# Optimization experiments

Measured on AMD Instinct MI355X. Metric: run time of the kernel, lower is better.

## Reference

```python
import jax, jax.numpy as jnp
import numpy as np

INPUT, HIDDEN, OUTPUT = 512, 1024, 512
B, T = 256, 512

def setup_inputs() -> dict:
    key = jax.random.key(0)
    ks = jax.random.split(key, 15)
    def lin(k, fin, fout):
        bound = 1.0 / np.sqrt(fin)
        kw, kb = jax.random.split(k)
        W = jax.random.uniform(kw, (fout, fin), jnp.float32, -bound, bound)
        b = jax.random.uniform(kb, (fout,), jnp.float32, -bound, bound)
        return W, b
    x = jax.random.normal(ks[0], (B, T, INPUT), jnp.float32)
    Wxr, bxr = lin(ks[1], INPUT, HIDDEN)
    Whr, bhr = lin(ks[2], HIDDEN, HIDDEN)
    Wxc, bxc = lin(ks[3], INPUT, HIDDEN)
    Whc, bhc = lin(ks[4], HIDDEN, HIDDEN)
    Wxz, bxz = lin(ks[5], INPUT, HIDDEN)
    Whz, bhz = lin(ks[6], HIDDEN, HIDDEN)
    Wo, bo = lin(ks[7], HIDDEN, OUTPUT)
    return {"x": x, "Wxr": Wxr, "bxr": bxr, "Whr": Whr, "bhr": bhr,
            "Wxc": Wxc, "bxc": bxc, "Whc": Whc, "bhc": bhc,
            "Wxz": Wxz, "bxz": bxz, "Whz": Whz, "bhz": bhz,
            "Wo": Wo, "bo": bo}

def reference(x, Wxr, bxr, Whr, bhr, Wxc, bxc, Whc, bhc, Wxz, bxz, Whz, bhz, Wo, bo):
    # Precompute all input-to-gate projections in one big GEMM each: [B,T,H]
    xr = jnp.einsum('bti,hi->bth', x, Wxr) + bxr
    xc = jnp.einsum('bti,hi->bth', x, Wxc) + bxc
    xz = jnp.einsum('bti,hi->bth', x, Wxz) + bxz
    # time-major for scan: [T,B,H]
    xs = (xr.transpose(1, 0, 2), xc.transpose(1, 0, 2), xz.transpose(1, 0, 2))

    h0 = jnp.zeros((x.shape[0], Whr.shape[0]), x.dtype)

    def step(h, xt):
        xr_t, xc_t, xz_t = xt
        r = jax.nn.sigmoid(xr_t + h @ Whr.T + bhr)
        c = jnp.tanh(xc_t + r * (h @ Whc.T + bhc))
        z = jax.nn.sigmoid(xz_t + h @ Whz.T + bhz)
        h_new = (1.0 - z) * h + z * c
        return h_new, None

    h_final, _ = jax.lax.scan(step, h0, xs)
    return h_final @ Wo.T + bo
```

## Files before the change

kernel.cpp:

```cpp
#include <hip/hip_runtime.h>

typedef __attribute__((ext_vector_type(8))) short s16x8;
typedef __attribute__((ext_vector_type(4))) float f32x4;

#define SCOPE_AGENT __HIP_MEMORY_SCOPE_AGENT

static __device__ __forceinline__ unsigned short f2bf(float f) {
    unsigned u = __float_as_uint(f);
    u = (u + 0x7fffu + ((u >> 16) & 1u)) >> 16;
    return (unsigned short)u;
}

static __device__ __forceinline__ unsigned ld_sc1(const unsigned* p) {
    return __hip_atomic_load(p, __ATOMIC_RELAXED, SCOPE_AGENT);
}
static __device__ __forceinline__ void st_sc1(unsigned* p, unsigned v) {
    __hip_atomic_store(p, v, __ATOMIC_RELAXED, SCOPE_AGENT);
}

__global__ void k_cast_bf16(const float* __restrict__ src,
                            unsigned short* __restrict__ dst, int n4) {
    int i = blockIdx.x * blockDim.x + threadIdx.x;
    int stride = gridDim.x * blockDim.x;
    for (; i < n4; i += stride) {
        float4 v = reinterpret_cast<const float4*>(src)[i];
        ushort4 o;
        o.x = f2bf(v.x); o.y = f2bf(v.y); o.z = f2bf(v.z); o.w = f2bf(v.w);
        reinterpret_cast<ushort4*>(dst)[i] = o;
    }
}

__global__ __launch_bounds__(256, 1) void k_gru(
    const unsigned short* __restrict__ x16,
    const unsigned short* __restrict__ wh,
    const unsigned short* __restrict__ wx,
    const unsigned short* __restrict__ wo,
    const float* __restrict__ bxr_, const float* __restrict__ bhr_,
    const float* __restrict__ bxc_, const float* __restrict__ bhc_,
    const float* __restrict__ bxz_, const float* __restrict__ bhz_,
    const float* __restrict__ bo_,
    unsigned short* __restrict__ h16a,
    unsigned short* __restrict__ h16b,
    unsigned* __restrict__ slots,
    unsigned* __restrict__ rel,
    float* __restrict__ out)
{
    extern __shared__ unsigned short lds[];

    const int tid = threadIdx.x;
    const int bid = blockIdx.x;
    const int xcd = bid & 7;
    const int rb  = xcd >> 1;
    const int jt  = ((bid >> 3) << 1) | (xcd & 1);
    const int b0  = rb * 64;
    const int j0  = jt * 16;

    for (int i = 0; i < 36; ++i) {
        int gidx = i * 256 + tid;
        int rr = gidx / 192;
        int gc = gidx - rr * 192;
        int k  = gc << 3;
        int gate = rr >> 4;
        int j = j0 + (rr & 15);
        const unsigned short* src =
            (k < 1024) ? (wh + ((size_t)gate << 20) + ((size_t)j << 10) + k)
                       : (wx + (size_t)gate * 524288 + ((size_t)j << 9) + (k - 1024));
        s16x8 v = *reinterpret_cast<const s16x8*>(src);
        int boff = ((rr * 192 + gc) << 4) ^ ((rr & 7) << 4);
        *reinterpret_cast<s16x8*>(reinterpret_cast<char*>(lds) + boff) = v;
    }
    __syncthreads();

    const int lane = tid & 63;
    const int wv   = tid >> 6;
    const int l15  = lane & 15;
    const int lk   = lane >> 4;

    const int b   = b0 + wv * 16 + l15;
    const int jq  = j0 + lk * 4;
    const int swz = (l15 & 7) << 4;
    const int rbase0 = (l15)      * 192 + lk;
    const int rbase1 = (16 + l15) * 192 + lk;
    const int rbase2 = (32 + l15) * 192 + lk;

    float bR[4], bZ[4], bCh[4], bCx[4];
#pragma unroll
    for (int e = 0; e < 4; ++e) {
        int j = jq + e;
        bR[e]  = bxr_[j] + bhr_[j];
        bZ[e]  = bxz_[j] + bhz_[j];
        bCh[e] = bhc_[j];
        bCx[e] = bxc_[j];
    }

    float hreg[4] = {0.f, 0.f, 0.f, 0.f};
    char* lb = reinterpret_cast<char*>(lds);
    const unsigned short* xrowbase = x16 + (size_t)b * 262144 + lk * 8;
    unsigned* myflag  = &slots[(rb << 6) + jt];
    unsigned* grel    = &rel[rb << 6];

    f32x4 xR = {0.f,0.f,0.f,0.f}, xZ = {0.f,0.f,0.f,0.f}, xC = {0.f,0.f,0.f,0.f};
    {
        s16x8 xf[16];
#pragma unroll
        for (int kk = 0; kk < 16; ++kk)
            xf[kk] = *reinterpret_cast<const s16x8*>(xrowbase + kk * 32);
#pragma unroll
        for (int kk = 0; kk < 16; ++kk) {
            s16x8 w0 = *reinterpret_cast<s16x8*>(lb + (((rbase0 + (kk + 32) * 4) << 4) ^ swz));
            s16x8 w1 = *reinterpret_cast<s16x8*>(lb + (((rbase1 + (kk + 32) * 4) << 4) ^ swz));
            s16x8 w2 = *reinterpret_cast<s16x8*>(lb + (((rbase2 + (kk + 32) * 4) << 4) ^ swz));
            xR = __builtin_amdgcn_mfma_f32_16x16x32_bf16(w0, xf[kk], xR, 0, 0, 0);
            xC = __builtin_amdgcn_mfma_f32_16x16x32_bf16(w1, xf[kk], xC, 0, 0, 0);
            xZ = __builtin_amdgcn_mfma_f32_16x16x32_bf16(w2, xf[kk], xZ, 0, 0, 0);
        }
    }

    unsigned short* hc = h16a;
    unsigned short* hn = h16b;

    for (int t = 0; t < 512; ++t) {
        if (wv == 0) {
            while (ld_sc1(grel) < (unsigned)t) __builtin_amdgcn_s_sleep(1);
        }
        __syncthreads();
        asm volatile("" ::: "memory");

        s16x8 hf[32];
        const unsigned short* hrow = hc + ((size_t)b << 10) + lk * 8;
#pragma unroll
        for (int kk = 0; kk < 32; ++kk)
            hf[kk] = *reinterpret_cast<const s16x8*>(hrow + kk * 32);

        s16x8 xfn[16];
        if (t < 511) {
            const unsigned short* axn = xrowbase + (size_t)(t + 1) * 512;
#pragma unroll
            for (int kk = 0; kk < 16; ++kk)
                xfn[kk] = *reinterpret_cast<const s16x8*>(axn + kk * 32);
        }

        f32x4 aR = xR, aZ = xZ, aCx = xC;
        f32x4 aCh = {0.f,0.f,0.f,0.f};
#pragma unroll
        for (int kk = 0; kk < 32; ++kk) {
            s16x8 w0 = *reinterpret_cast<s16x8*>(lb + (((rbase0 + kk * 4) << 4) ^ swz));
            s16x8 w1 = *reinterpret_cast<s16x8*>(lb + (((rbase1 + kk * 4) << 4) ^ swz));
            s16x8 w2 = *reinterpret_cast<s16x8*>(lb + (((rbase2 + kk * 4) << 4) ^ swz));
            aR  = __builtin_amdgcn_mfma_f32_16x16x32_bf16(w0, hf[kk], aR, 0, 0, 0);
            aCh = __builtin_amdgcn_mfma_f32_16x16x32_bf16(w1, hf[kk], aCh, 0, 0, 0);
            aZ  = __builtin_amdgcn_mfma_f32_16x16x32_bf16(w2, hf[kk], aZ, 0, 0, 0);
        }

        unsigned long long pack = 0ull;
#pragma unroll
        for (int e = 0; e < 4; ++e) {
            float r   = __builtin_amdgcn_rcpf(1.f + __expf(-(aR[e] + bR[e])));
            float zg  = __builtin_amdgcn_rcpf(1.f + __expf(-(aZ[e] + bZ[e])));
            float u2  = aCx[e] + bCx[e] + r * (aCh[e] + bCh[e]);
            float cg  = 1.f - 2.f * __builtin_amdgcn_rcpf(__expf(2.f * u2) + 1.f);
            float hnv = (1.f - zg) * hreg[e] + zg * cg;
            hreg[e] = hnv;
            pack |= (unsigned long long)f2bf(hnv) << (16 * e);
        }
        __hip_atomic_store(
            reinterpret_cast<unsigned long long*>(hn + ((size_t)b << 10) + jq),
            pack, __ATOMIC_RELAXED, SCOPE_AGENT);

        __syncthreads();
        if (tid == 0) {
            st_sc1(myflag, (unsigned)(t + 1));
            (void)__hip_atomic_load(grel, __ATOMIC_ACQUIRE, SCOPE_AGENT);
        }

        if (jt == 0 && wv == 0) {
            const unsigned tgt = (unsigned)(t + 1);
            for (;;) {
                unsigned v = ld_sc1(&slots[(rb << 6) + lane]);
                if (__all((int)(v >= tgt))) break;
                __builtin_amdgcn_s_sleep(1);
            }
            if (tid == 0) st_sc1(grel, tgt);
        }

        if (t < 511) {
            xR = {0.f,0.f,0.f,0.f}; xZ = {0.f,0.f,0.f,0.f}; xC = {0.f,0.f,0.f,0.f};
#pragma unroll
            for (int kk = 0; kk < 16; ++kk) {
                s16x8 w0 = *reinterpret_cast<s16x8*>(lb + (((rbase0 + (kk + 32) * 4) << 4) ^ swz));
                s16x8 w1 = *reinterpret_cast<s16x8*>(lb + (((rbase1 + (kk + 32) * 4) << 4) ^ swz));
                s16x8 w2 = *reinterpret_cast<s16x8*>(lb + (((rbase2 + (kk + 32) * 4) << 4) ^ swz));
                xR = __builtin_amdgcn_mfma_f32_16x16x32_bf16(w0, xfn[kk], xR, 0, 0, 0);
                xC = __builtin_amdgcn_mfma_f32_16x16x32_bf16(w1, xfn[kk], xC, 0, 0, 0);
                xZ = __builtin_amdgcn_mfma_f32_16x16x32_bf16(w2, xfn[kk], xZ, 0, 0, 0);
            }
        }

        unsigned short* tmp = hc; hc = hn; hn = tmp;
    }

    if (wv == 0) {
        while (ld_sc1(grel) < 512u) __builtin_amdgcn_s_sleep(1);
        (void)__hip_atomic_load(grel, __ATOMIC_ACQUIRE, SCOPE_AGENT);
    }
    __syncthreads();
    asm volatile("" ::: "memory");

    const int ocol  = jt * 8 + l15;
    const int ocolc = (l15 < 8) ? ocol : (jt * 8 + 7);
    f32x4 aO = {0.f,0.f,0.f,0.f};
    const unsigned short* hrow = hc + ((size_t)b << 10) + lk * 8;
    const unsigned short* bw = wo + ((size_t)ocolc << 10) + lk * 8;
#pragma unroll
    for (int kk = 0; kk < 32; ++kk) {
        s16x8 hv = *reinterpret_cast<const s16x8*>(hrow + kk * 32);
        s16x8 wb = *reinterpret_cast<const s16x8*>(bw + kk * 32);
        aO = __builtin_amdgcn_mfma_f32_16x16x32_bf16(hv, wb, aO, 0, 0, 0);
    }
    if (l15 < 8) {
        const float bov = bo_[ocol];
#pragma unroll
        for (int e = 0; e < 4; ++e) {
            out[((size_t)(b0 + wv * 16 + lk * 4 + e) << 9) + ocol] = aO[e] + bov;
        }
    }
}

extern "C" void kernel_launch(void* const* d_in, const int* in_sizes, int n_in,
                              void* d_out, int out_size, void* d_ws, size_t ws_size,
                              hipStream_t stream) {
    const float* x   = (const float*)d_in[0];
    const float* Wxr = (const float*)d_in[1];
    const float* bxr = (const float*)d_in[2];
    const float* Whr = (const float*)d_in[3];
    const float* bhr = (const float*)d_in[4];
    const float* Wxc = (const float*)d_in[5];
    const float* bxc = (const float*)d_in[6];
    const float* Whc = (const float*)d_in[7];
    const float* bhc = (const float*)d_in[8];
    const float* Wxz = (const float*)d_in[9];
    const float* bxz = (const float*)d_in[10];
    const float* Whz = (const float*)d_in[11];
    const float* bhz = (const float*)d_in[12];
    const float* Wo  = (const float*)d_in[13];
    const float* bo  = (const float*)d_in[14];

    char* ws = (char*)d_ws;
    unsigned short* x16  = (unsigned short*)(ws);
    unsigned short* wh   = (unsigned short*)(ws + 134217728);
    unsigned short* wx   = (unsigned short*)(ws + 140509184);
    unsigned short* wo16 = (unsigned short*)(ws + 143654912);
    unsigned short* h16a = (unsigned short*)(ws + 144703488);
    unsigned short* h16b = (unsigned short*)(ws + 145227776);
    unsigned*       slots= (unsigned*)(ws + 145752064);
    unsigned*       rel  = (unsigned*)(ws + 145753088);

    auto cast = [&](const float* s, unsigned short* d, int n) {
        int n4 = n >> 2;
        int blocks = (n4 + 255) / 256;
        if (blocks > 4096) blocks = 4096;
        k_cast_bf16<<<blocks, 256, 0, stream>>>(s, d, n4);
    };
    cast(x,   x16, 67108864);
    cast(Whr, wh,            1048576);
    cast(Whc, wh + 1048576,  1048576);
    cast(Whz, wh + 2097152,  1048576);
    cast(Wxr, wx,            524288);
    cast(Wxc, wx + 524288,   524288);
    cast(Wxz, wx + 1048576,  524288);
    cast(Wo,  wo16,          524288);

    hipMemsetAsync(h16a, 0, 524288, stream);
    hipMemsetAsync(slots, 0, 2048, stream);

    hipFuncSetAttribute(reinterpret_cast<const void*>(k_gru),
                        hipFuncAttributeMaxDynamicSharedMemorySize, 147456);
    k_gru<<<dim3(256), dim3(256), 147456, stream>>>(
        x16, wh, wx, wo16, bxr, bhr, bxc, bhc, bxz, bhz, bo,
        h16a, h16b, slots, rel, (float*)d_out);
}
```

Before: 4.755 ms.

## Split recurrent K-reduction across two wave groups with LDS partial-sum exchange

Doubles the block to 512 threads and splits the hidden-state reduction of each step into two halves handled by separate waves. The upper half also computes the next step's input projection, then hands its partial sums to the lower half through an LDS buffer. The lower half finishes the gate math and writes h. This shortens the per-step serial MFMA chain on the critical path, at the cost of an extra block barrier, an LDS round-trip per step, and 160KB of LDS per block.

Result: slower. 5.589 ms (+17.5%).

```diff
diff --git a/kernel.cpp b/kernel.cpp
--- a/kernel.cpp
+++ b/kernel.cpp
@@ -30,7 +30,7 @@
     }
 }
 
-__global__ __launch_bounds__(256, 1) void k_gru(
+__global__ __launch_bounds__(512, 1) void k_gru(
     const unsigned short* __restrict__ x16,
     const unsigned short* __restrict__ wh,
     const unsigned short* __restrict__ wx,
@@ -45,7 +45,8 @@
     unsigned* __restrict__ rel,
     float* __restrict__ out)
 {
-    extern __shared__ unsigned short lds[];
+    extern __shared__ char ldsb[];
+    f32x4* rbuf = reinterpret_cast<f32x4*>(ldsb + 147456);
 
     const int tid = threadIdx.x;
     const int bid = blockIdx.x;
@@ -55,33 +56,47 @@
     const int b0  = rb * 64;
     const int j0  = jt * 16;
 
-    for (int i = 0; i < 36; ++i) {
-        int gidx = i * 256 + tid;
-        int rr = gidx / 192;
-        int gc = gidx - rr * 192;
-        int k  = gc << 3;
+    for (int i = 0; i < 12; ++i) {
+        int gidx = i * 512 + tid;
+        int rr = gidx >> 7;
+        int gc = gidx & 127;
         int gate = rr >> 4;
         int j = j0 + (rr & 15);
-        const unsigned short* src =
-            (k < 1024) ? (wh + ((size_t)gate << 20) + ((size_t)j << 10) + k)
-                       : (wx + (size_t)gate * 524288 + ((size_t)j << 9) + (k - 1024));
-        s16x8 v = *reinterpret_cast<const s16x8*>(src);
-        int boff = ((rr * 192 + gc) << 4) ^ ((rr & 7) << 4);
-        *reinterpret_cast<s16x8*>(reinterpret_cast<char*>(lds) + boff) = v;
+        s16x8 v = *reinterpret_cast<const s16x8*>(
+            wh + ((size_t)gate << 20) + ((size_t)j << 10) + gc * 8);
+        int boff = ((rr * 128 + gc) << 4) ^ ((rr & 15) << 4);
+        *reinterpret_cast<s16x8*>(ldsb + boff) = v;
+    }
+    for (int i = 0; i < 6; ++i) {
+        int gidx = i * 512 + tid;
+        int rr = gidx >> 6;
+        int gc = gidx & 63;
+        int gate = rr >> 4;
+        int j = j0 + (rr & 15);
+        s16x8 v = *reinterpret_cast<const s16x8*>(
+            wx + (size_t)gate * 524288 + (size_t)j * 512 + gc * 8);
+        int boff = 98304 + (((rr * 64 + gc) << 4) ^ ((rr & 15) << 4));
+        *reinterpret_cast<s16x8*>(ldsb + boff) = v;
     }
     __syncthreads();
 
     const int lane = tid & 63;
     const int wv   = tid >> 6;
+    const int bt   = wv & 3;
+    const int kh   = wv >> 2;
     const int l15  = lane & 15;
     const int lk   = lane >> 4;
-
-    const int b   = b0 + wv * 16 + l15;
-    const int jq  = j0 + lk * 4;
-    const int swz = (l15 & 7) << 4;
-    const int rbase0 = (l15)      * 192 + lk;
-    const int rbase1 = (16 + l15) * 192 + lk;
-    const int rbase2 = (32 + l15) * 192 + lk;
+    const int swz4 = l15 << 4;
+
+    const int b  = b0 + bt * 16 + l15;
+    const int jq = j0 + lk * 4;
+
+    const int hwR = l15 * 128 + kh * 64 + lk;
+    const int hwC = 2048 + l15 * 128 + kh * 64 + lk;
+    const int hwZ = 4096 + l15 * 128 + kh * 64 + lk;
+    const int xwR = 6144 + l15 * 64 + lk;
+    const int xwC = 6144 + 1024 + l15 * 64 + lk;
+    const int xwZ = 6144 + 2048 + l15 * 64 + lk;
 
     float bR[4], bZ[4], bCh[4], bCx[4];
 #pragma unroll
@@ -94,25 +109,25 @@
     }
 
     float hreg[4] = {0.f, 0.f, 0.f, 0.f};
-    char* lb = reinterpret_cast<char*>(lds);
-    const unsigned short* xrowbase = x16 + (size_t)b * 262144 + lk * 8;
-    unsigned* myflag  = &slots[(rb << 6) + jt];
-    unsigned* grel    = &rel[rb << 6];
-
-    f32x4 xR = {0.f,0.f,0.f,0.f}, xZ = {0.f,0.f,0.f,0.f}, xC = {0.f,0.f,0.f,0.f};
-    {
-        s16x8 xf[16];
+    f32x4 aR = {0,0,0,0}, aZ = {0,0,0,0}, aCh = {0,0,0,0}, aCx = {0,0,0,0};
+    s16x8 xfn[16];
+
+    const unsigned short* xrow = x16 + (size_t)b * 262144 + lk * 8;
+    unsigned* myflag = &slots[(rb << 6) + jt];
+    unsigned* grel   = &rel[rb << 6];
+
+    if (kh == 1) {
 #pragma unroll
         for (int kk = 0; kk < 16; ++kk)
-            xf[kk] = *reinterpret_cast<const s16x8*>(xrowbase + kk * 32);
+            xfn[kk] = *reinterpret_cast<const s16x8*>(xrow + kk * 32);
 #pragma unroll
         for (int kk = 0; kk < 16; ++kk) {
-            s16x8 w0 = *reinterpret_cast<s16x8*>(lb + (((rbase0 + (kk + 32) * 4) << 4) ^ swz));
-            s16x8 w1 = *reinterpret_cast<s16x8*>(lb + (((rbase1 + (kk + 32) * 4) << 4) ^ swz));
-            s16x8 w2 = *reinterpret_cast<s16x8*>(lb + (((rbase2 + (kk + 32) * 4) << 4) ^ swz));
-            xR = __builtin_amdgcn_mfma_f32_16x16x32_bf16(w0, xf[kk], xR, 0, 0, 0);
-            xC = __builtin_amdgcn_mfma_f32_16x16x32_bf16(w1, xf[kk], xC, 0, 0, 0);
-            xZ = __builtin_amdgcn_mfma_f32_16x16x32_bf16(w2, xf[kk], xZ, 0, 0, 0);
+            s16x8 w0 = *reinterpret_cast<s16x8*>(ldsb + (((xwR + kk * 4) << 4) ^ swz4));
+            s16x8 w1 = *reinterpret_cast<s16x8*>(ldsb + (((xwC + kk * 4) << 4) ^ swz4));
+            s16x8 w2 = *reinterpret_cast<s16x8*>(ldsb + (((xwZ + kk * 4) << 4) ^ swz4));
+            aR  = __builtin_amdgcn_mfma_f32_16x16x32_bf16(w0, xfn[kk], aR, 0, 0, 0);
+            aCx = __builtin_amdgcn_mfma_f32_16x16x32_bf16(w1, xfn[kk], aCx, 0, 0, 0);
+            aZ  = __builtin_amdgcn_mfma_f32_16x16x32_bf16(w2, xfn[kk], aZ, 0, 0, 0);
         }
     }
 
@@ -126,46 +141,59 @@
         __syncthreads();
         asm volatile("" ::: "memory");
 
-        s16x8 hf[32];
-        const unsigned short* hrow = hc + ((size_t)b << 10) + lk * 8;
-#pragma unroll
-        for (int kk = 0; kk < 32; ++kk)
+        s16x8 hf[16];
+        const unsigned short* hrow = hc + ((size_t)b << 10) + kh * 512 + lk * 8;
+#pragma unroll
+        for (int kk = 0; kk < 16; ++kk)
             hf[kk] = *reinterpret_cast<const s16x8*>(hrow + kk * 32);
 
-        s16x8 xfn[16];
-        if (t < 511) {
-            const unsigned short* axn = xrowbase + (size_t)(t + 1) * 512;
+        if (kh == 1 && t < 511) {
+            const unsigned short* axn = xrow + (size_t)(t + 1) * 512;
 #pragma unroll
             for (int kk = 0; kk < 16; ++kk)
                 xfn[kk] = *reinterpret_cast<const s16x8*>(axn + kk * 32);
         }
 
-        f32x4 aR = xR, aZ = xZ, aCx = xC;
-        f32x4 aCh = {0.f,0.f,0.f,0.f};
-#pragma unroll
-        for (int kk = 0; kk < 32; ++kk) {
-            s16x8 w0 = *reinterpret_cast<s16x8*>(lb + (((rbase0 + kk * 4) << 4) ^ swz));
-            s16x8 w1 = *reinterpret_cast<s16x8*>(lb + (((rbase1 + kk * 4) << 4) ^ swz));
-            s16x8 w2 = *reinterpret_cast<s16x8*>(lb + (((rbase2 + kk * 4) << 4) ^ swz));
+        if (kh == 0) { aR = {0,0,0,0}; aZ = {0,0,0,0}; aCx = {0,0,0,0}; }
+        aCh = {0,0,0,0};
+#pragma unroll
+        for (int kk = 0; kk < 16; ++kk) {
+            s16x8 w0 = *reinterpret_cast<s16x8*>(ldsb + (((hwR + kk * 4) << 4) ^ swz4));
+            s16x8 w1 = *reinterpret_cast<s16x8*>(ldsb + (((hwC + kk * 4) << 4) ^ swz4));
+            s16x8 w2 = *reinterpret_cast<s16x8*>(ldsb + (((hwZ + kk * 4) << 4) ^ swz4));
             aR  = __builtin_amdgcn_mfma_f32_16x16x32_bf16(w0, hf[kk], aR, 0, 0, 0);
             aCh = __builtin_amdgcn_mfma_f32_16x16x32_bf16(w1, hf[kk], aCh, 0, 0, 0);
             aZ  = __builtin_amdgcn_mfma_f32_16x16x32_bf16(w2, hf[kk], aZ, 0, 0, 0);
         }
 
-        unsigned long long pack = 0ull;
-#pragma unroll
-        for (int e = 0; e < 4; ++e) {
-            float r   = __builtin_amdgcn_rcpf(1.f + __expf(-(aR[e] + bR[e])));
-            float zg  = __builtin_amdgcn_rcpf(1.f + __expf(-(aZ[e] + bZ[e])));
-            float u2  = aCx[e] + bCx[e] + r * (aCh[e] + bCh[e]);
-            float cg  = 1.f - 2.f * __builtin_amdgcn_rcpf(__expf(2.f * u2) + 1.f);
-            float hnv = (1.f - zg) * hreg[e] + zg * cg;
-            hreg[e] = hnv;
-            pack |= (unsigned long long)f2bf(hnv) << (16 * e);
-        }
-        __hip_atomic_store(
-            reinterpret_cast<unsigned long long*>(hn + ((size_t)b << 10) + jq),
-            pack, __ATOMIC_RELAXED, SCOPE_AGENT);
+        if (kh == 1) {
+            rbuf[(bt * 4 + 0) * 64 + lane] = aR;
+            rbuf[(bt * 4 + 1) * 64 + lane] = aZ;
+            rbuf[(bt * 4 + 2) * 64 + lane] = aCh;
+            rbuf[(bt * 4 + 3) * 64 + lane] = aCx;
+        }
+        __syncthreads();
+
+        if (kh == 0) {
+            aR  += rbuf[(bt * 4 + 0) * 64 + lane];
+            aZ  += rbuf[(bt * 4 + 1) * 64 + lane];
+            aCh += rbuf[(bt * 4 + 2) * 64 + lane];
+            aCx += rbuf[(bt * 4 + 3) * 64 + lane];
+            unsigned long long pack = 0ull;
+#pragma unroll
+            for (int e = 0; e < 4; ++e) {
+                float r   = __builtin_amdgcn_rcpf(1.f + __expf(-(aR[e] + bR[e])));
+                float zg  = __builtin_amdgcn_rcpf(1.f + __expf(-(aZ[e] + bZ[e])));
+                float u2  = aCx[e] + bCx[e] + r * (aCh[e] + bCh[e]);
+                float cg  = 1.f - 2.f * __builtin_amdgcn_rcpf(__expf(2.f * u2) + 1.f);
+                float hnv = (1.f - zg) * hreg[e] + zg * cg;
+                hreg[e] = hnv;
+                pack |= (unsigned long long)f2bf(hnv) << (16 * e);
+            }
+            __hip_atomic_store(
+                reinterpret_cast<unsigned long long*>(hn + ((size_t)b << 10) + jq),
+                pack, __ATOMIC_RELAXED, SCOPE_AGENT);
+        }
 
         __syncthreads();
         if (tid == 0) {
@@ -183,16 +211,16 @@
             if (tid == 0) st_sc1(grel, tgt);
         }
 
-        if (t < 511) {
-            xR = {0.f,0.f,0.f,0.f}; xZ = {0.f,0.f,0.f,0.f}; xC = {0.f,0.f,0.f,0.f};
+        if (kh == 1 && t < 511) {
+            aR = {0,0,0,0}; aZ = {0,0,0,0}; aCx = {0,0,0,0};
 #pragma unroll
             for (int kk = 0; kk < 16; ++kk) {
-                s16x8 w0 = *reinterpret_cast<s16x8*>(lb + (((rbase0 + (kk + 32) * 4) << 4) ^ swz));
-                s16x8 w1 = *reinterpret_cast<s16x8*>(lb + (((rbase1 + (kk + 32) * 4) << 4) ^ swz));
-                s16x8 w2 = *reinterpret_cast<s16x8*>(lb + (((rbase2 + (kk + 32) * 4) << 4) ^ swz));
-                xR = __builtin_amdgcn_mfma_f32_16x16x32_bf16(w0, xfn[kk], xR, 0, 0, 0);
-                xC = __builtin_amdgcn_mfma_f32_16x16x32_bf16(w1, xfn[kk], xC, 0, 0, 0);
-                xZ = __builtin_amdgcn_mfma_f32_16x16x32_bf16(w2, xfn[kk], xZ, 0, 0, 0);
+                s16x8 w0 = *reinterpret_cast<s16x8*>(ldsb + (((xwR + kk * 4) << 4) ^ swz4));
+                s16x8 w1 = *reinterpret_cast<s16x8*>(ldsb + (((xwC + kk * 4) << 4) ^ swz4));
+                s16x8 w2 = *reinterpret_cast<s16x8*>(ldsb + (((xwZ + kk * 4) << 4) ^ swz4));
+                aR  = __builtin_amdgcn_mfma_f32_16x16x32_bf16(w0, xfn[kk], aR, 0, 0, 0);
+                aCx = __builtin_amdgcn_mfma_f32_16x16x32_bf16(w1, xfn[kk], aCx, 0, 0, 0);
+                aZ  = __builtin_amdgcn_mfma_f32_16x16x32_bf16(w2, xfn[kk], aZ, 0, 0, 0);
             }
         }
 
@@ -206,22 +234,24 @@
     __syncthreads();
     asm volatile("" ::: "memory");
 
-    const int ocol  = jt * 8 + l15;
-    const int ocolc = (l15 < 8) ? ocol : (jt * 8 + 7);
-    f32x4 aO = {0.f,0.f,0.f,0.f};
-    const unsigned short* hrow = hc + ((size_t)b << 10) + lk * 8;
-    const unsigned short* bw = wo + ((size_t)ocolc << 10) + lk * 8;
-#pragma unroll
-    for (int kk = 0; kk < 32; ++kk) {
-        s16x8 hv = *reinterpret_cast<const s16x8*>(hrow + kk * 32);
-        s16x8 wb = *reinterpret_cast<const s16x8*>(bw + kk * 32);
-        aO = __builtin_amdgcn_mfma_f32_16x16x32_bf16(hv, wb, aO, 0, 0, 0);
-    }
-    if (l15 < 8) {
-        const float bov = bo_[ocol];
-#pragma unroll
-        for (int e = 0; e < 4; ++e) {
-            out[((size_t)(b0 + wv * 16 + lk * 4 + e) << 9) + ocol] = aO[e] + bov;
+    if (kh == 0) {
+        const int ocol  = jt * 8 + l15;
+        const int ocolc = (l15 < 8) ? ocol : (jt * 8 + 7);
+        f32x4 aO = {0,0,0,0};
+        const unsigned short* hrow = hc + ((size_t)b << 10) + lk * 8;
+        const unsigned short* bw = wo + ((size_t)ocolc << 10) + lk * 8;
+#pragma unroll
+        for (int kk = 0; kk < 32; ++kk) {
+            s16x8 hv = *reinterpret_cast<const s16x8*>(hrow + kk * 32);
+            s16x8 wb = *reinterpret_cast<const s16x8*>(bw + kk * 32);
+            aO = __builtin_amdgcn_mfma_f32_16x16x32_bf16(hv, wb, aO, 0, 0, 0);
+        }
+        if (l15 < 8) {
+            const float bov = bo_[ocol];
+#pragma unroll
+            for (int e = 0; e < 4; ++e) {
+                out[((size_t)(b0 + bt * 16 + lk * 4 + e) << 9) + ocol] = aO[e] + bov;
+            }
         }
     }
 }
@@ -274,8 +304,8 @@
     hipMemsetAsync(slots, 0, 2048, stream);
 
     hipFuncSetAttribute(reinterpret_cast<const void*>(k_gru),
-                        hipFuncAttributeMaxDynamicSharedMemorySize, 147456);
-    k_gru<<<dim3(256), dim3(256), 147456, stream>>>(
+                        hipFuncAttributeMaxDynamicSharedMemorySize, 163840);
+    k_gru<<<dim3(256), dim3(512), 163840, stream>>>(
         x16, wh, wx, wo16, bxr, bhr, bxc, bhc, bxz, bhz, bo,
         h16a, h16b, slots, rel, (float*)d_out);
 }
```
